# Kernel optimization log

Measured on AMD Instinct MI355X. Metric: run time of the kernel, lower is better.

The kernel has to match this reference:

```python
import jax, jax.numpy as jnp
import numpy as np

N_HEADS = 8
D_EMBED = 512
D_HEAD = D_EMBED // N_HEADS
BS, SEQ = 2, 4096


def setup_inputs() -> dict:
    key = jax.random.key(0)
    ks = jax.random.split(key, 9)
    s = 1.0 / np.sqrt(D_EMBED)
    inp = {
        "x": jax.random.normal(ks[0], (BS, SEQ, D_EMBED), dtype=jnp.float32),
        "wq": jax.random.uniform(ks[1], (D_EMBED, D_EMBED), jnp.float32, -s, s),
        "bq": jax.random.uniform(ks[2], (D_EMBED,), jnp.float32, -s, s),
        "wk": jax.random.uniform(ks[3], (D_EMBED, D_EMBED), jnp.float32, -s, s),
        "bk": jax.random.uniform(ks[4], (D_EMBED,), jnp.float32, -s, s),
        "wv": jax.random.uniform(ks[5], (D_EMBED, D_EMBED), jnp.float32, -s, s),
        "bv": jax.random.uniform(ks[6], (D_EMBED,), jnp.float32, -s, s),
        "wo": jax.random.uniform(ks[7], (D_EMBED, D_EMBED), jnp.float32, -s, s),
        "bo": jax.random.uniform(ks[8], (D_EMBED,), jnp.float32, -s, s),
        "causal_mask": 1,
    }
    return inp


def reference(x, wq, bq, wk, bk, wv, bv, wo, bo, causal_mask):
    bs, seq, d = x.shape
    # torch Linear: y = x @ W^T + b, then SiLU gate
    q = jax.nn.silu(jnp.einsum('bsd,ed->bse', x, wq) + bq)
    k = jax.nn.silu(jnp.einsum('bsd,ed->bse', x, wk) + bk)
    v = jax.nn.silu(jnp.einsum('bsd,ed->bse', x, wv) + bv)
    # split heads: [b, h, s, dh]
    q = q.reshape(bs, seq, N_HEADS, D_HEAD).transpose(0, 2, 1, 3)
    k = k.reshape(bs, seq, N_HEADS, D_HEAD).transpose(0, 2, 1, 3)
    v = v.reshape(bs, seq, N_HEADS, D_HEAD).transpose(0, 2, 1, 3)
    scores = jnp.einsum('bhqd,bhkd->bhqk', q, k)  # [b,h,s,s]
    if causal_mask:
        mask = jnp.triu(jnp.ones((seq, seq), dtype=bool), k=1)
        scores = jnp.where(mask, -jnp.inf, scores)
    scores = scores / jnp.sqrt(jnp.asarray(D_HEAD, dtype=scores.dtype))
    attn = jax.nn.softmax(scores, axis=-1)
    out = jnp.einsum('bhqk,bhkd->bhqd', attn, v)
    out = out.transpose(0, 2, 1, 3).reshape(bs, seq, d)
    return jnp.einsum('bsd,ed->bse', out, wo) + bo
```

## Files before the change

### kernel.cpp

```cpp
#include <hip/hip_runtime.h>
#include <stdint.h>


typedef float  f32x4  __attribute__((ext_vector_type(4)));
typedef float  f32x16 __attribute__((ext_vector_type(16)));
typedef short  bf16x8 __attribute__((ext_vector_type(8)));
typedef unsigned int u32x4 __attribute__((ext_vector_type(4)));

#define DEV static __device__ __forceinline__

#define BSZ   2
#define SEQL  4096
#define NHEAD 8
#define DHEAD 64
#define DEMB  512
#define MROWS (BSZ*SEQL)
#define NXE   (MROWS*DEMB)
#define NWE   (DEMB*DEMB)

DEV void async_copy16(const void* g, void* l) {
  __builtin_amdgcn_global_load_lds(
      (const __attribute__((address_space(1))) void*)g,
      (__attribute__((address_space(3))) void*)l,
      16, 0, 0);
}

DEV unsigned short f2bf_bits(float f) {
  unsigned int x = __float_as_uint(f);
  x = x + 0x7FFFu + ((x >> 16) & 1u);
  return (unsigned short)(x >> 16);
}

__global__ __launch_bounds__(256) void convert_all(
    const float* __restrict__ x,
    const float* __restrict__ wq, const float* __restrict__ wk,
    const float* __restrict__ wv, const float* __restrict__ wo,
    unsigned short* __restrict__ dst)
{
  const int nch = (NXE + 4 * NWE) / 4;
  for (int c = blockIdx.x * 256 + threadIdx.x; c < nch; c += gridDim.x * 256) {
    const int off = c * 4;
    const float* src;
    int rel;
    if (off < NXE) {
      src = x; rel = off;
    } else {
      int rr = off - NXE;
      int j = rr >> 18;
      rel = rr & (NWE - 1);
      src = (j == 0) ? wq : (j == 1) ? wk : (j == 2) ? wv : wo;
    }
    float4 v = *(const float4*)(src + rel);
    ushort4 o = make_ushort4(f2bf_bits(v.x), f2bf_bits(v.y),
                             f2bf_bits(v.z), f2bf_bits(v.w));
    *(ushort4*)(dst + off) = o;
  }
}

DEV void gemm_mainloop64(const unsigned short* __restrict__ A,
                         const unsigned short* __restrict__ B,
                         int arow0, int brow0,
                         unsigned short* Ash, unsigned short* Bsh,
                         int t, f32x4 acc[4][2])
{
  const int l = t & 63;
  const int w = t >> 6, wr = w >> 1, wc = w & 1;
  for (int kt = 0; kt < 8; ++kt) {
    const int k0 = kt * 64;
#pragma unroll
    for (int i = 0; i < 4; ++i) {
      int p = t + i * 256;
      int r = p >> 3;
      int c0 = ((p & 7) ^ (r & 7)) * 8;
      async_copy16(A + (size_t)(arow0 + r) * DEMB + k0 + c0, (char*)Ash + p * 16);
    }
#pragma unroll
    for (int i = 0; i < 2; ++i) {
      int p = t + i * 256;
      int r = p >> 3;
      int c0 = ((p & 7) ^ (r & 7)) * 8;
      async_copy16(B + (size_t)(brow0 + r) * DEMB + k0 + c0, (char*)Bsh + p * 16);
    }
    __syncthreads();

    bf16x8 af[4][2], bf[2][2];
#pragma unroll
    for (int m = 0; m < 4; ++m)
#pragma unroll
      for (int ks = 0; ks < 2; ++ks) {
        int r = wr * 64 + m * 16 + (l & 15);
        int c = (ks * 4 + (l >> 4)) ^ (r & 7);
        af[m][ks] = *(const bf16x8*)((const char*)Ash + r * 128 + c * 16);
      }
#pragma unroll
    for (int n = 0; n < 2; ++n)
#pragma unroll
      for (int ks = 0; ks < 2; ++ks) {
        int r = wc * 32 + n * 16 + (l & 15);
        int c = (ks * 4 + (l >> 4)) ^ (r & 7);
        bf[n][ks] = *(const bf16x8*)((const char*)Bsh + r * 128 + c * 16);
      }
#pragma unroll
    for (int m = 0; m < 4; ++m)
#pragma unroll
      for (int n = 0; n < 2; ++n)
#pragma unroll
        for (int ks = 0; ks < 2; ++ks)
          acc[m][n] = __builtin_amdgcn_mfma_f32_16x16x32_bf16(
              af[m][ks], bf[n][ks], acc[m][n], 0, 0, 0);
    __syncthreads();
  }
}

__global__ __launch_bounds__(256) void qkv_gemm(
    const unsigned short* __restrict__ xb,
    const unsigned short* __restrict__ wqb,
    const unsigned short* __restrict__ wkb,
    const unsigned short* __restrict__ wvb,
    const float* __restrict__ bq, const float* __restrict__ bk,
    const float* __restrict__ bv,
    unsigned short* __restrict__ q_out,
    unsigned short* __restrict__ k_out,
    unsigned short* __restrict__ v_out)
{
  __shared__ unsigned short Ash[128 * 64];
  __shared__ unsigned short Bsh[64 * 64];
  const int z = blockIdx.z;
  const unsigned short* W = (z == 0) ? wqb : (z == 1) ? wkb : wvb;
  const float* bias = (z == 0) ? bq : (z == 1) ? bk : bv;
  unsigned short* dst = (z == 0) ? q_out : (z == 1) ? k_out : v_out;

  f32x4 acc[4][2];
#pragma unroll
  for (int m = 0; m < 4; ++m)
#pragma unroll
    for (int n = 0; n < 2; ++n) acc[m][n] = (f32x4){0.f, 0.f, 0.f, 0.f};

  gemm_mainloop64(xb, W, blockIdx.x * 128, blockIdx.y * 64, Ash, Bsh,
                  threadIdx.x, acc);

  const int t = threadIdx.x, l = t & 63, w = t >> 6, wr = w >> 1, wc = w & 1;
  const float qscale = (z == 0) ? 0.18033688011112042f : 1.0f;
#pragma unroll
  for (int n = 0; n < 2; ++n) {
    const int e = blockIdx.y * 64 + wc * 32 + n * 16 + (l & 15);
    const float bval = bias[e];
    const int h = e >> 6, d = e & 63;
#pragma unroll
    for (int m = 0; m < 4; ++m)
#pragma unroll
      for (int g = 0; g < 4; ++g) {
        const int R = blockIdx.x * 128 + wr * 64 + m * 16 + (l >> 4) * 4 + g;
        float v = acc[m][n][g] + bval;
        v = v / (1.0f + __expf(-v));
        v *= qscale;
        const int b = R >> 12, s = R & 4095;
        const int head = b * NHEAD + h;
        size_t off;
        if (z == 1) {
          const int kt = s >> 5, ql = s & 31;
          const int dt = d >> 4, hi = (d >> 3) & 1, ee = d & 7;
          const int lane = (hi << 5) | ql;
          off = (size_t)head * (SEQL * DHEAD) +
                (size_t)(((kt << 2) + dt) << 9) + (lane << 3) + ee;
        } else {
          off = (((size_t)head) * SEQL + s) * DHEAD + d;
        }
        dst[off] = f2bf_bits(v);
      }
  }
}

__global__ __launch_bounds__(256) void vtrans(
    const unsigned short* __restrict__ vb, unsigned short* __restrict__ vtb)
{
  __shared__ unsigned short tile[64 * 66];
  const int t = threadIdx.x;
  const int bh = blockIdx.y;
  const int s0 = blockIdx.x * 64;
#pragma unroll
  for (int i = 0; i < 2; ++i) {
    int p = t + i * 256;
    int r = p >> 3, c0 = (p & 7) * 8;
    bf16x8 v = *(const bf16x8*)(vb + ((size_t)bh * SEQL + s0 + r) * DHEAD + c0);
#pragma unroll
    for (int j = 0; j < 8; ++j) tile[r * 66 + c0 + j] = (unsigned short)v[j];
  }
  __syncthreads();
#pragma unroll
  for (int i = 0; i < 2; ++i) {
    int p = t + i * 256;
    int dh = p >> 3, c0 = (p & 7) * 8;
    bf16x8 o;
#pragma unroll
    for (int j = 0; j < 8; ++j) o[j] = (short)tile[(c0 + j) * 66 + dh];
    const int sb = s0 + c0;
    const int kt = sb >> 5, rem = sb & 31;
    const int hf = rem >> 4, hi = (rem >> 3) & 1;
    const int n = dh >> 5, ql = dh & 31;
    const int lane = (hi << 5) | ql;
    const size_t off = (size_t)bh * (SEQL * DHEAD) +
        (size_t)((((kt << 1) + n) << 1) + hf) * 512 + (lane << 3);
    *(bf16x8*)(vtb + off) = o;
  }
}

__global__ __launch_bounds__(256) void attn_fwd(
    const unsigned short* __restrict__ qb,
    const unsigned short* __restrict__ kfb,
    const unsigned short* __restrict__ vfb,
    unsigned short* __restrict__ attnb,
    const int* __restrict__ causal_ptr)
{
  __shared__ float Osh[2][32][65];
  __shared__ float Lsh[2][32];

  const int t = threadIdx.x;
  const int l = t & 63;
  const int ql = l & 31;
  const int hi = l >> 5;
  const int wid = t >> 6;
  const int r = wid & 1;
  const int h = wid >> 1;
  const int bid = blockIdx.x;
  const int cc = bid & 255, qq = bid >> 8;
  const int g = cc >> 4;
  const int head = cc & 15;
  const int j = (qq == 0) ? (63 - g) : (qq == 1) ? g
              : (qq == 2) ? (47 - g) : (16 + g);
  const int q0w = j * 64 + r * 32;
  const int causal = causal_ptr[0];

  const unsigned short* qbase = qb + (size_t)head * SEQL * DHEAD;
  const unsigned short* kbase = kfb + (size_t)head * SEQL * DHEAD;
  const unsigned short* vbase = vfb + (size_t)head * SEQL * DHEAD;

  bf16x8 qf[4];
#pragma unroll
  for (int dt = 0; dt < 4; ++dt)
    qf[dt] = *(const bf16x8*)(qbase +
        (unsigned)((q0w + ql) * DHEAD + dt * 16 + hi * 8));

  f32x16 o0, o1;
#pragma unroll
  for (int i = 0; i < 16; ++i) { o0[i] = 0.f; o1[i] = 0.f; }
  float rl = 0.f;

  const int T = causal ? 2 * (j + 1) : (SEQL / 32);
  const int ktm = (T + 1) >> 1;
  const int kt0 = h ? ktm : 0;
  const int kt1 = h ? T : ktm;

  const unsigned l8 = (unsigned)(l << 3);

  for (int kt = kt0; kt < kt1; ++kt) {
    const int k0 = kt * 32;

    const unsigned short* kp = kbase + ((unsigned)(kt << 2) << 9) + l8;
    bf16x8 kf[4];
#pragma unroll
    for (int dt = 0; dt < 4; ++dt)
      kf[dt] = *(const bf16x8*)(kp + (dt << 9));

    const unsigned short* vp = vbase + ((unsigned)(kt << 2) << 9) + l8;
    bf16x8 vf[2][2];
#pragma unroll
    for (int n = 0; n < 2; ++n)
#pragma unroll
      for (int hf = 0; hf < 2; ++hf)
        vf[n][hf] = *(const bf16x8*)(vp + (((n << 1) + hf) << 9));

    f32x16 s;
#pragma unroll
    for (int i = 0; i < 16; ++i) s[i] = 0.f;
#pragma unroll
    for (int dt = 0; dt < 4; ++dt)
      s = __builtin_amdgcn_mfma_f32_32x32x16_bf16(kf[dt], qf[dt], s, 0, 0, 0);

    if (causal && (k0 + 31 > q0w)) {
      const int qrow = q0w + ql;
#pragma unroll
      for (int rg = 0; rg < 16; ++rg) {
        const int kk = k0 + (rg & 3) + 8 * (rg >> 2) + 4 * hi;
        s[rg] = (kk > qrow) ? -1e30f : s[rg];
      }
    }

#pragma unroll
    for (int rg = 0; rg < 16; ++rg)
      s[rg] = __builtin_amdgcn_exp2f(s[rg]);

    rl += (((s[0] + s[1]) + (s[2] + s[3])) + ((s[4] + s[5]) + (s[6] + s[7])))
        + (((s[8] + s[9]) + (s[10] + s[11])) + ((s[12] + s[13]) + (s[14] + s[15])));

#pragma unroll
    for (int hf = 0; hf < 2; ++hf) {
      const int b8 = hf * 8;
      float e0 = s[b8 + 0], e1 = s[b8 + 1], e2 = s[b8 + 2], e3 = s[b8 + 3];
      float e4 = s[b8 + 4], e5 = s[b8 + 5], e6 = s[b8 + 6], e7 = s[b8 + 7];
      unsigned a0, a1, b0, b1;
      asm("v_cvt_pk_bf16_f32 %0, %1, %2" : "=v"(a0) : "v"(e0), "v"(e1));
      asm("v_cvt_pk_bf16_f32 %0, %1, %2" : "=v"(a1) : "v"(e2), "v"(e3));
      asm("v_cvt_pk_bf16_f32 %0, %1, %2" : "=v"(b0) : "v"(e4), "v"(e5));
      asm("v_cvt_pk_bf16_f32 %0, %1, %2" : "=v"(b1) : "v"(e6), "v"(e7));
      asm("v_permlane32_swap_b32 %0, %1" : "+v"(a0), "+v"(b0));
      asm("v_permlane32_swap_b32 %0, %1" : "+v"(a1), "+v"(b1));
      u32x4 pau = {a0, a1, b0, b1};
      bf16x8 pa = *(bf16x8*)&pau;
      o0 = __builtin_amdgcn_mfma_f32_32x32x16_bf16(pa, vf[0][hf], o0, 0, 0, 0);
      o1 = __builtin_amdgcn_mfma_f32_32x32x16_bf16(pa, vf[1][hf], o1, 0, 0, 0);
    }
  }

  rl += __shfl_xor(rl, 32);

  if (h == 1) {
#pragma unroll
    for (int rg = 0; rg < 16; ++rg) {
      const int cr = (rg & 3) + 8 * (rg >> 2) + 4 * hi;
      Osh[r][cr][ql] = o0[rg];
      Osh[r][cr][32 + ql] = o1[rg];
    }
    if (l < 32) Lsh[r][l] = rl;
  }
  __syncthreads();
  if (h == 0) {
    const float inv = 1.0f / (rl + Lsh[r][ql]);
    const int b2 = head >> 3, hh = head & 7;
#pragma unroll
    for (int rg = 0; rg < 16; ++rg) {
      const int cr = (rg & 3) + 8 * (rg >> 2) + 4 * hi;
      const float invr = __shfl(inv, cr);
      const int srow = q0w + cr;
      const float v0 = (o0[rg] + Osh[r][cr][ql]) * invr;
      const float v1 = (o1[rg] + Osh[r][cr][32 + ql]) * invr;
      unsigned short* dst = attnb + ((size_t)b2 * SEQL + srow) * DEMB + hh * DHEAD;
      dst[ql] = f2bf_bits(v0);
      dst[32 + ql] = f2bf_bits(v1);
    }
  }
}

__global__ __launch_bounds__(256) void out_gemm(
    const unsigned short* __restrict__ ab,
    const unsigned short* __restrict__ wob,
    const float* __restrict__ bo,
    float* __restrict__ out)
{
  __shared__ unsigned short Ash[128 * 64];
  __shared__ unsigned short Bsh[64 * 64];
  f32x4 acc[4][2];
#pragma unroll
  for (int m = 0; m < 4; ++m)
#pragma unroll
    for (int n = 0; n < 2; ++n) acc[m][n] = (f32x4){0.f, 0.f, 0.f, 0.f};

  gemm_mainloop64(ab, wob, blockIdx.x * 128, blockIdx.y * 64, Ash, Bsh,
                  threadIdx.x, acc);

  const int t = threadIdx.x, l = t & 63, w = t >> 6, wr = w >> 1, wc = w & 1;
#pragma unroll
  for (int n = 0; n < 2; ++n) {
    const int e = blockIdx.y * 64 + wc * 32 + n * 16 + (l & 15);
    const float bval = bo[e];
#pragma unroll
    for (int m = 0; m < 4; ++m)
#pragma unroll
      for (int g = 0; g < 4; ++g) {
        const int R = blockIdx.x * 128 + wr * 64 + m * 16 + (l >> 4) * 4 + g;
        out[(size_t)R * DEMB + e] = acc[m][n][g] + bval;
      }
  }
}

extern "C" void kernel_launch(void* const* d_in, const int* in_sizes, int n_in,
                              void* d_out, int out_size, void* d_ws, size_t ws_size,
                              hipStream_t stream)
{
  const float* x  = (const float*)d_in[0];
  const float* wq = (const float*)d_in[1];
  const float* bq = (const float*)d_in[2];
  const float* wk = (const float*)d_in[3];
  const float* bk = (const float*)d_in[4];
  const float* wv = (const float*)d_in[5];
  const float* bv = (const float*)d_in[6];
  const float* wo = (const float*)d_in[7];
  const float* bo = (const float*)d_in[8];
  const int* causal = (const int*)d_in[9];
  float* out = (float*)d_out;

  unsigned short* ws  = (unsigned short*)d_ws;
  unsigned short* xb  = ws;
  unsigned short* wqb = xb + NXE;
  unsigned short* wkb = wqb + NWE;
  unsigned short* wvb = wkb + NWE;
  unsigned short* wob = wvb + NWE;
  unsigned short* qb  = wob + NWE;
  unsigned short* kfb = qb + NXE;
  unsigned short* vb2 = kfb + NXE;
  unsigned short* vfb = vb2 + NXE;
  unsigned short* atb = vfb + NXE;

  convert_all<<<dim3(1024), dim3(256), 0, stream>>>(x, wq, wk, wv, wo, xb);
  qkv_gemm<<<dim3(64, 8, 3), dim3(256), 0, stream>>>(
      xb, wqb, wkb, wvb, bq, bk, bv, qb, kfb, vb2);
  vtrans<<<dim3(64, 16), dim3(256), 0, stream>>>(vb2, vfb);
  attn_fwd<<<dim3(1024), dim3(256), 0, stream>>>(qb, kfb, vfb, atb, causal);
  out_gemm<<<dim3(64, 8), dim3(256), 0, stream>>>(atb, wob, bo, out);
}
```

Baseline: 100.8 us.

## Split each 32-row query tile's KV range across four waves with tree reduction

Each block now handles one 32-row query tile instead of two, and its four waves each process a quarter of the key range, with partial outputs combined through shared memory in a two-step tree reduction. The grid doubles to 2048 blocks. The causal tile count is now per 32-row tile, so the second half of each 64-row tile no longer processes an extra fully masked key tile. The goal is finer-grained parallelism and better load balance, at the cost of more shared-memory reduction steps and barriers per block and each wave loading its own Q fragments.

```diff
diff --git a/kernel.cpp b/kernel.cpp
--- a/kernel.cpp
+++ b/kernel.cpp
@@ -219,15 +219,15 @@
   const int l = t & 63;
   const int ql = l & 31;
   const int hi = l >> 5;
-  const int wid = t >> 6;
-  const int r = wid & 1;
-  const int h = wid >> 1;
+  const int e = t >> 6;
   const int bid = blockIdx.x;
   const int cc = bid & 255, qq = bid >> 8;
   const int g = cc >> 4;
   const int head = cc & 15;
-  const int j = (qq == 0) ? (63 - g) : (qq == 1) ? g
-              : (qq == 2) ? (47 - g) : (16 + g);
+  const int jsel = qq & 3;
+  const int j = (jsel == 0) ? (63 - g) : (jsel == 1) ? g
+              : (jsel == 2) ? (47 - g) : (16 + g);
+  const int r = qq >> 2;
   const int q0w = j * 64 + r * 32;
   const int causal = causal_ptr[0];
 
@@ -246,10 +246,9 @@
   for (int i = 0; i < 16; ++i) { o0[i] = 0.f; o1[i] = 0.f; }
   float rl = 0.f;
 
-  const int T = causal ? 2 * (j + 1) : (SEQL / 32);
-  const int ktm = (T + 1) >> 1;
-  const int kt0 = h ? ktm : 0;
-  const int kt1 = h ? T : ktm;
+  const int T = causal ? (2 * j + r + 1) : (SEQL / 32);
+  const int kt0 = (T * e) >> 2;
+  const int kt1 = (T * (e + 1)) >> 2;
 
   const unsigned l8 = (unsigned)(l << 3);
 
@@ -314,26 +313,56 @@
 
   rl += __shfl_xor(rl, 32);
 
-  if (h == 1) {
+  if (e == 1 || e == 3) {
+    const int buf = e >> 1;
 #pragma unroll
     for (int rg = 0; rg < 16; ++rg) {
       const int cr = (rg & 3) + 8 * (rg >> 2) + 4 * hi;
-      Osh[r][cr][ql] = o0[rg];
-      Osh[r][cr][32 + ql] = o1[rg];
-    }
-    if (l < 32) Lsh[r][l] = rl;
+      Osh[buf][cr][ql] = o0[rg];
+      Osh[buf][cr][32 + ql] = o1[rg];
+    }
+    if (l < 32) Lsh[buf][l] = rl;
   }
   __syncthreads();
-  if (h == 0) {
-    const float inv = 1.0f / (rl + Lsh[r][ql]);
+  if (e == 0 || e == 2) {
+    const int buf = e >> 1;
+#pragma unroll
+    for (int rg = 0; rg < 16; ++rg) {
+      const int cr = (rg & 3) + 8 * (rg >> 2) + 4 * hi;
+      o0[rg] += Osh[buf][cr][ql];
+      o1[rg] += Osh[buf][cr][32 + ql];
+    }
+    rl += Lsh[buf][ql];
+  }
+  __syncthreads();
+  if (e == 2) {
+#pragma unroll
+    for (int rg = 0; rg < 16; ++rg) {
+      const int cr = (rg & 3) + 8 * (rg >> 2) + 4 * hi;
+      Osh[0][cr][ql] = o0[rg];
+      Osh[0][cr][32 + ql] = o1[rg];
+    }
+    if (l < 32) Lsh[0][l] = rl;
+  }
+  __syncthreads();
+  if (e == 0) {
+#pragma unroll
+    for (int rg = 0; rg < 16; ++rg) {
+      const int cr = (rg & 3) + 8 * (rg >> 2) + 4 * hi;
+      o0[rg] += Osh[0][cr][ql];
+      o1[rg] += Osh[0][cr][32 + ql];
+    }
+    rl += Lsh[0][ql];
+
+    const float inv = 1.0f / rl;
     const int b2 = head >> 3, hh = head & 7;
 #pragma unroll
     for (int rg = 0; rg < 16; ++rg) {
       const int cr = (rg & 3) + 8 * (rg >> 2) + 4 * hi;
       const float invr = __shfl(inv, cr);
       const int srow = q0w + cr;
-      const float v0 = (o0[rg] + Osh[r][cr][ql]) * invr;
-      const float v1 = (o1[rg] + Osh[r][cr][32 + ql]) * invr;
+      const float v0 = o0[rg] * invr;
+      const float v1 = o1[rg] * invr;
       unsigned short* dst = attnb + ((size_t)b2 * SEQL + srow) * DEMB + hh * DHEAD;
       dst[ql] = f2bf_bits(v0);
       dst[32 + ql] = f2bf_bits(v1);
@@ -405,6 +434,6 @@
   qkv_gemm<<<dim3(64, 8, 3), dim3(256), 0, stream>>>(
       xb, wqb, wkb, wvb, bq, bk, bv, qb, kfb, vb2);
   vtrans<<<dim3(64, 16), dim3(256), 0, stream>>>(vb2, vfb);
-  attn_fwd<<<dim3(1024), dim3(256), 0, stream>>>(qb, kfb, vfb, atb, causal);
+  attn_fwd<<<dim3(2048), dim3(256), 0, stream>>>(qb, kfb, vfb, atb, causal);
   out_gemm<<<dim3(64, 8), dim3(256), 0, stream>>>(atb, wob, bo, out);
 }
```

Result: slower. 106.9 us (+6.0%).

## Process two 32-row query tiles per wave to reuse K/V fragment loads

Applied to the files above, without the earlier changes.

Each wave now handles 64 query rows (two 32-row MFMA tiles) instead of 32, so each K and V fragment loaded from global memory feeds two score and PV MFMA chains. The block covers 128 query rows, the grid is halved to 512 blocks, and the causal work-pairing scheme is simplified to two blocks per query-block pair. The aim is to cut global K/V load traffic per unit of compute. In exchange it raises register pressure with doubled accumulators and Q fragments, uses more shared memory, and leaves fewer blocks for load balancing across CUs.

```diff
diff --git a/kernel.cpp b/kernel.cpp
--- a/kernel.cpp
+++ b/kernel.cpp
@@ -212,42 +212,47 @@
     unsigned short* __restrict__ attnb,
     const int* __restrict__ causal_ptr)
 {
-  __shared__ float Osh[2][32][65];
-  __shared__ float Lsh[2][32];
+  __shared__ float Osh[2][64][65];
+  __shared__ float Lsh[2][64];
 
   const int t = threadIdx.x;
   const int l = t & 63;
   const int ql = l & 31;
   const int hi = l >> 5;
   const int wid = t >> 6;
-  const int r = wid & 1;
-  const int h = wid >> 1;
+  const int r2 = wid & 1;
+  const int h  = wid >> 1;
   const int bid = blockIdx.x;
   const int cc = bid & 255, qq = bid >> 8;
   const int g = cc >> 4;
   const int head = cc & 15;
-  const int j = (qq == 0) ? (63 - g) : (qq == 1) ? g
-              : (qq == 2) ? (47 - g) : (16 + g);
-  const int q0w = j * 64 + r * 32;
+  const int J = qq ? g : (31 - g);
+  const int q0 = J * 128 + r2 * 64;
   const int causal = causal_ptr[0];
 
   const unsigned short* qbase = qb + (size_t)head * SEQL * DHEAD;
   const unsigned short* kbase = kfb + (size_t)head * SEQL * DHEAD;
   const unsigned short* vbase = vfb + (size_t)head * SEQL * DHEAD;
 
-  bf16x8 qf[4];
-#pragma unroll
-  for (int dt = 0; dt < 4; ++dt)
-    qf[dt] = *(const bf16x8*)(qbase +
-        (unsigned)((q0w + ql) * DHEAD + dt * 16 + hi * 8));
-
-  f32x16 o0, o1;
-#pragma unroll
-  for (int i = 0; i < 16; ++i) { o0[i] = 0.f; o1[i] = 0.f; }
-  float rl = 0.f;
-
-  const int T = causal ? 2 * (j + 1) : (SEQL / 32);
-  const int ktm = (T + 1) >> 1;
+  bf16x8 qf[2][4];
+#pragma unroll
+  for (int rt = 0; rt < 2; ++rt)
+#pragma unroll
+    for (int dt = 0; dt < 4; ++dt)
+      qf[rt][dt] = *(const bf16x8*)(qbase +
+          (unsigned)((q0 + rt * 32 + ql) * DHEAD + dt * 16 + hi * 8));
+
+  f32x16 o[2][2];
+  float rl[2] = {0.f, 0.f};
+#pragma unroll
+  for (int rt = 0; rt < 2; ++rt)
+#pragma unroll
+    for (int n = 0; n < 2; ++n)
+#pragma unroll
+      for (int i = 0; i < 16; ++i) o[rt][n][i] = 0.f;
+
+  const int T = causal ? (4 * J + 2 * r2 + 2) : (SEQL / 32);
+  const int ktm = T >> 1;
   const int kt0 = h ? ktm : 0;
   const int kt1 = h ? T : ktm;
 
@@ -270,73 +275,85 @@
       for (int hf = 0; hf < 2; ++hf)
         vf[n][hf] = *(const bf16x8*)(vp + (((n << 1) + hf) << 9));
 
-    f32x16 s;
-#pragma unroll
-    for (int i = 0; i < 16; ++i) s[i] = 0.f;
-#pragma unroll
-    for (int dt = 0; dt < 4; ++dt)
-      s = __builtin_amdgcn_mfma_f32_32x32x16_bf16(kf[dt], qf[dt], s, 0, 0, 0);
-
-    if (causal && (k0 + 31 > q0w)) {
-      const int qrow = q0w + ql;
+#pragma unroll
+    for (int rt = 0; rt < 2; ++rt) {
+      const int q0w = q0 + rt * 32;
+      if (causal && k0 > q0w + 31) continue;
+
+      f32x16 s;
+#pragma unroll
+      for (int i = 0; i < 16; ++i) s[i] = 0.f;
+#pragma unroll
+      for (int dt = 0; dt < 4; ++dt)
+        s = __builtin_amdgcn_mfma_f32_32x32x16_bf16(kf[dt], qf[rt][dt], s, 0, 0, 0);
+
+      if (causal && (k0 + 31 > q0w)) {
+        const int qrow = q0w + ql;
+#pragma unroll
+        for (int rg = 0; rg < 16; ++rg) {
+          const int kk = k0 + (rg & 3) + 8 * (rg >> 2) + 4 * hi;
+          s[rg] = (kk > qrow) ? -1e30f : s[rg];
+        }
+      }
+
+#pragma unroll
+      for (int rg = 0; rg < 16; ++rg)
+        s[rg] = __builtin_amdgcn_exp2f(s[rg]);
+
+      rl[rt] += (((s[0] + s[1]) + (s[2] + s[3])) + ((s[4] + s[5]) + (s[6] + s[7])))
+              + (((s[8] + s[9]) + (s[10] + s[11])) + ((s[12] + s[13]) + (s[14] + s[15])));
+
+#pragma unroll
+      for (int hf = 0; hf < 2; ++hf) {
+        const int b8 = hf * 8;
+        float e0 = s[b8 + 0], e1 = s[b8 + 1], e2 = s[b8 + 2], e3 = s[b8 + 3];
+        float e4 = s[b8 + 4], e5 = s[b8 + 5], e6 = s[b8 + 6], e7 = s[b8 + 7];
+        unsigned a0, a1, b0, b1;
+        asm("v_cvt_pk_bf16_f32 %0, %1, %2" : "=v"(a0) : "v"(e0), "v"(e1));
+        asm("v_cvt_pk_bf16_f32 %0, %1, %2" : "=v"(a1) : "v"(e2), "v"(e3));
+        asm("v_cvt_pk_bf16_f32 %0, %1, %2" : "=v"(b0) : "v"(e4), "v"(e5));
+        asm("v_cvt_pk_bf16_f32 %0, %1, %2" : "=v"(b1) : "v"(e6), "v"(e7));
+        asm("v_permlane32_swap_b32 %0, %1" : "+v"(a0), "+v"(b0));
+        asm("v_permlane32_swap_b32 %0, %1" : "+v"(a1), "+v"(b1));
+        u32x4 pau = {a0, a1, b0, b1};
+        bf16x8 pa = *(bf16x8*)&pau;
+        o[rt][0] = __builtin_amdgcn_mfma_f32_32x32x16_bf16(pa, vf[0][hf], o[rt][0], 0, 0, 0);
+        o[rt][1] = __builtin_amdgcn_mfma_f32_32x32x16_bf16(pa, vf[1][hf], o[rt][1], 0, 0, 0);
+      }
+    }
+  }
+
+  rl[0] += __shfl_xor(rl[0], 32);
+  rl[1] += __shfl_xor(rl[1], 32);
+
+  if (h == 1) {
+#pragma unroll
+    for (int rt = 0; rt < 2; ++rt)
 #pragma unroll
       for (int rg = 0; rg < 16; ++rg) {
-        const int kk = k0 + (rg & 3) + 8 * (rg >> 2) + 4 * hi;
-        s[rg] = (kk > qrow) ? -1e30f : s[rg];
-      }
-    }
-
-#pragma unroll
-    for (int rg = 0; rg < 16; ++rg)
-      s[rg] = __builtin_amdgcn_exp2f(s[rg]);
-
-    rl += (((s[0] + s[1]) + (s[2] + s[3])) + ((s[4] + s[5]) + (s[6] + s[7])))
-        + (((s[8] + s[9]) + (s[10] + s[11])) + ((s[12] + s[13]) + (s[14] + s[15])));
-
-#pragma unroll
-    for (int hf = 0; hf < 2; ++hf) {
-      const int b8 = hf * 8;
-      float e0 = s[b8 + 0], e1 = s[b8 + 1], e2 = s[b8 + 2], e3 = s[b8 + 3];
-      float e4 = s[b8 + 4], e5 = s[b8 + 5], e6 = s[b8 + 6], e7 = s[b8 + 7];
-      unsigned a0, a1, b0, b1;
-      asm("v_cvt_pk_bf16_f32 %0, %1, %2" : "=v"(a0) : "v"(e0), "v"(e1));
-      asm("v_cvt_pk_bf16_f32 %0, %1, %2" : "=v"(a1) : "v"(e2), "v"(e3));
-      asm("v_cvt_pk_bf16_f32 %0, %1, %2" : "=v"(b0) : "v"(e4), "v"(e5));
-      asm("v_cvt_pk_bf16_f32 %0, %1, %2" : "=v"(b1) : "v"(e6), "v"(e7));
-      asm("v_permlane32_swap_b32 %0, %1" : "+v"(a0), "+v"(b0));
-      asm("v_permlane32_swap_b32 %0, %1" : "+v"(a1), "+v"(b1));
-      u32x4 pau = {a0, a1, b0, b1};
-      bf16x8 pa = *(bf16x8*)&pau;
-      o0 = __builtin_amdgcn_mfma_f32_32x32x16_bf16(pa, vf[0][hf], o0, 0, 0, 0);
-      o1 = __builtin_amdgcn_mfma_f32_32x32x16_bf16(pa, vf[1][hf], o1, 0, 0, 0);
-    }
-  }
-
-  rl += __shfl_xor(rl, 32);
-
-  if (h == 1) {
-#pragma unroll
-    for (int rg = 0; rg < 16; ++rg) {
-      const int cr = (rg & 3) + 8 * (rg >> 2) + 4 * hi;
-      Osh[r][cr][ql] = o0[rg];
-      Osh[r][cr][32 + ql] = o1[rg];
-    }
-    if (l < 32) Lsh[r][l] = rl;
+        const int cr = (rg & 3) + 8 * (rg >> 2) + 4 * hi;
+        Osh[r2][rt * 32 + cr][ql] = o[rt][0][rg];
+        Osh[r2][rt * 32 + cr][32 + ql] = o[rt][1][rg];
+      }
+    if (l < 32) { Lsh[r2][l] = rl[0]; Lsh[r2][32 + l] = rl[1]; }
   }
   __syncthreads();
   if (h == 0) {
-    const float inv = 1.0f / (rl + Lsh[r][ql]);
     const int b2 = head >> 3, hh = head & 7;
 #pragma unroll
-    for (int rg = 0; rg < 16; ++rg) {
-      const int cr = (rg & 3) + 8 * (rg >> 2) + 4 * hi;
-      const float invr = __shfl(inv, cr);
-      const int srow = q0w + cr;
-      const float v0 = (o0[rg] + Osh[r][cr][ql]) * invr;
-      const float v1 = (o1[rg] + Osh[r][cr][32 + ql]) * invr;
-      unsigned short* dst = attnb + ((size_t)b2 * SEQL + srow) * DEMB + hh * DHEAD;
-      dst[ql] = f2bf_bits(v0);
-      dst[32 + ql] = f2bf_bits(v1);
+    for (int rt = 0; rt < 2; ++rt) {
+      const float inv = 1.0f / (rl[rt] + Lsh[r2][rt * 32 + ql]);
+#pragma unroll
+      for (int rg = 0; rg < 16; ++rg) {
+        const int cr = (rg & 3) + 8 * (rg >> 2) + 4 * hi;
+        const float invr = __shfl(inv, cr);
+        const int srow = q0 + rt * 32 + cr;
+        const float v0 = (o[rt][0][rg] + Osh[r2][rt * 32 + cr][ql]) * invr;
+        const float v1 = (o[rt][1][rg] + Osh[r2][rt * 32 + cr][32 + ql]) * invr;
+        unsigned short* dst = attnb + ((size_t)b2 * SEQL + srow) * DEMB + hh * DHEAD;
+        dst[ql] = f2bf_bits(v0);
+        dst[32 + ql] = f2bf_bits(v1);
+      }
     }
   }
 }
@@ -405,6 +422,6 @@
   qkv_gemm<<<dim3(64, 8, 3), dim3(256), 0, stream>>>(
       xb, wqb, wkb, wvb, bq, bk, bv, qb, kfb, vb2);
   vtrans<<<dim3(64, 16), dim3(256), 0, stream>>>(vb2, vfb);
-  attn_fwd<<<dim3(1024), dim3(256), 0, stream>>>(qb, kfb, vfb, atb, causal);
+  attn_fwd<<<dim3(512), dim3(256), 0, stream>>>(qb, kfb, vfb, atb, causal);
   out_gemm<<<dim3(64, 8), dim3(256), 0, stream>>>(atb, wob, bo, out);
 }
```

Result: slower. 117.7 us (+16.7%).
